# Kernel optimization log

Measured on AMD Instinct MI355X. Metric: run time of the kernel, lower is better.

## Reference

```python
import jax, jax.numpy as jnp
import numpy as np

N = 50000      # nodes
E = 800000     # edges
F = 128        # node feature dim (= output_size, residual)
H = 128        # hidden_size

def _uniform_fan_avg(key, shape):
    # VarianceScaling(scale=1.0, mode='fan_avg', distribution='uniform')
    fan_avg = (shape[0] + shape[1]) / 2.0
    limit = np.sqrt(3.0 / fan_avg)
    return jax.random.uniform(key, shape, jnp.float32, -limit, limit)

def setup_inputs() -> dict:
    key = jax.random.key(0)
    ks = jax.random.split(key, 16)
    h = jax.random.normal(ks[0], (N, F), jnp.float32)
    pos = jax.random.normal(ks[1], (N, 3), jnp.float32)
    senders = jax.random.randint(ks[2], (E,), 0, N, jnp.int32)
    receivers = jax.random.randint(ks[3], (E,), 0, N, jnp.int32)
    # edge_mlp: Linear(2F+1 -> H) silu, Linear(H -> H) silu (activate_final=True)
    eW1 = _uniform_fan_avg(ks[4], (2 * F + 1, H)); eb1 = jnp.zeros((H,), jnp.float32)
    eW2 = _uniform_fan_avg(ks[5], (H, H)); eb2 = jnp.zeros((H,), jnp.float32)
    # node_mlp: Linear(F+H -> H) silu, Linear(H -> F) (no final act)
    nW1 = _uniform_fan_avg(ks[6], (F + H, H)); nb1 = jnp.zeros((H,), jnp.float32)
    nW2 = _uniform_fan_avg(ks[7], (H, F)); nb2 = jnp.zeros((F,), jnp.float32)
    # pos_correction_mlp: Linear(H -> H) silu, Linear(H -> 1, no bias, UniformScaling(dt))
    pW1 = _uniform_fan_avg(ks[8], (H, H)); pb1 = jnp.zeros((H,), jnp.float32)
    dt = 0.001
    pW2 = jax.random.uniform(ks[9], (H, 1), jnp.float32, -dt, dt) * np.sqrt(3.0)
    return {"h": h, "pos": pos, "senders": senders, "receivers": receivers,
            "eW1": eW1, "eb1": eb1, "eW2": eW2, "eb2": eb2,
            "nW1": nW1, "nb1": nb1, "nW2": nW2, "nb2": nb2,
            "pW1": pW1, "pb1": pb1, "pW2": pW2}

def reference(h, pos, senders, receivers,
              eW1, eb1, eW2, eb2,
              nW1, nb1, nW2, nb2,
              pW1, pb1, pW2):
    n = h.shape[0]
    # _coord2radial (normalize=False)
    coord_diff = pos[senders] - pos[receivers]            # [E,3]
    radial = jnp.sum(coord_diff ** 2, axis=1, keepdims=True)  # [E,1]
    # edge update (_message): concat(h[senders], h[receivers], radial) -> edge_mlp
    msg_in = jnp.concatenate([h[senders], h[receivers], radial], axis=-1)  # [E,2F+1]
    msg = jax.nn.silu(msg_in @ eW1 + eb1)
    msg = jax.nn.silu(msg @ eW2 + eb2)                    # [E,H]
    # node update (_update): aggregate messages at receivers, node_mlp, residual
    agg = jax.ops.segment_sum(msg, receivers, num_segments=n)  # [N,H]
    x = jnp.concatenate([h, agg], axis=-1)                # [N,F+H]
    x = jax.nn.silu(x @ nW1 + nb1)
    x = x @ nW2 + nb2                                     # [N,F]
    h_new = h + x                                         # residual
    # position update (_pos_update)
    pc = jax.nn.silu(msg @ pW1 + pb1) @ pW2               # [E,1]
    trans = jnp.clip(coord_diff * pc, -100, 100)          # [E,3]
    pos_new = pos + jax.ops.segment_sum(trans, senders, num_segments=n)
    return h_new, pos_new
```

## Files before the change

### kernel.cpp

```cpp
#include <hip/hip_runtime.h>
#include <hip/hip_bf16.h>

#define NNODES 50000
#define NEDGES 800000
#define EB 1024
#define SCAN_BLOCKS 196
#define TRN_BLOCKS 448

typedef short bf16x8 __attribute__((ext_vector_type(8)));
typedef float f32x4 __attribute__((ext_vector_type(4)));
typedef unsigned short u16;
typedef unsigned int u32;

__device__ __forceinline__ u16 f2bf(float f) {
    __hip_bfloat16 b = __float2bfloat16(f);
    return *reinterpret_cast<u16*>(&b);
}
__device__ __forceinline__ float bf2f(u16 v) {
    u32 u = ((u32)v) << 16;
    return __uint_as_float(u);
}
__device__ __forceinline__ u32 pack2(float a, float b) {
    __hip_bfloat162 t = __float22bfloat162_rn(float2{a, b});
    return *reinterpret_cast<u32*>(&t);
}
__device__ __forceinline__ float fast_silu(float x) {
    float e = __builtin_amdgcn_exp2f(-1.442695040888963f * x);
    return x * __builtin_amdgcn_rcpf(1.0f + e);
}
__device__ __forceinline__ bf16x8 ld8(const u16* p) {
    return *(const bf16x8*)p;
}
__device__ __forceinline__ f32x4 mfma16(bf16x8 a, bf16x8 b, f32x4 c) {
    return __builtin_amdgcn_mfma_f32_16x16x32_bf16(a, b, c, 0, 0, 0);
}

__global__ void prep_kernel(const float* __restrict__ eW1, const float* __restrict__ eW2,
                            const float* __restrict__ pW1, const float* __restrict__ nW1,
                            const float* __restrict__ nW2,
                            u16* __restrict__ eW1T, u16* __restrict__ eW2T,
                            u16* __restrict__ pW1T, u16* __restrict__ nW1T,
                            u16* __restrict__ nW2T,
                            const int* __restrict__ rcv, int* __restrict__ counts) {
    int b = blockIdx.x;
    if (b < TRN_BLOCKS) {
        int i = b * 256 + threadIdx.x;
        const float* src; u16* dst; int K;
        if (i < 32768)      { src = eW1; dst = eW1T; K = 256; }
        else if (i < 49152) { src = eW2; dst = eW2T; K = 128; i -= 32768; }
        else if (i < 65536) { src = pW1; dst = pW1T; K = 128; i -= 49152; }
        else if (i < 98304) { src = nW1; dst = nW1T; K = 256; i -= 65536; }
        else                { src = nW2; dst = nW2T; K = 128; i -= 98304; }
        int n = i / K, k = i - n * K;
        dst[i] = f2bf(src[k * 128 + n]);
    } else {
        int e = (b - TRN_BLOCKS) * 256 + threadIdx.x;
        if (e < NEDGES) atomicAdd(&counts[rcv[e]], 1);
    }
}

__global__ __launch_bounds__(256) void gemm_p(
    const float* __restrict__ h, const u16* __restrict__ eW1T,
    const u16* __restrict__ nW1T, const float* __restrict__ eb1,
    u16* __restrict__ P)
{
    const int tid  = threadIdx.x;
    const int w    = tid >> 6;
    const int lane = tid & 63;
    const int m    = lane & 15;
    const int quad = lane >> 4;
    const int ksub = quad * 8;

    bf16x8 bw[4][6];
    float bias[6];
    #pragma unroll
    for (int cc = 0; cc < 6; cc++) {
        int C = 96 * w + 16 * cc + m;
        const u16* bp;
        if (C < 128)      { bp = eW1T + C * 256;               bias[cc] = 0.5f * eb1[C]; }
        else if (C < 256) { bp = eW1T + (C - 128) * 256 + 128; bias[cc] = 0.5f * eb1[C - 128]; }
        else              { bp = nW1T + (C - 256) * 256;       bias[cc] = 0.f; }
        #pragma unroll
        for (int t = 0; t < 4; t++) bw[t][cc] = ld8(bp + t * 32 + ksub);
    }
    const int base = blockIdx.x * 64;
    #pragma unroll
    for (int mt = 0; mt < 4; mt++) {
        int nm = base + mt * 16 + m;
        if (nm >= NNODES) nm = NNODES - 1;
        bf16x8 afr[4];
        #pragma unroll
        for (int t = 0; t < 4; t++) {
            const float* ap = h + (size_t)nm * 128 + t * 32 + ksub;
            f32x4 lo = *(const f32x4*)ap;
            f32x4 hi = *(const f32x4*)(ap + 4);
            #pragma unroll
            for (int j = 0; j < 4; j++) {
                afr[t][j]     = (short)f2bf(lo[j]);
                afr[t][4 + j] = (short)f2bf(hi[j]);
            }
        }
        f32x4 acc[6];
        #pragma unroll
        for (int cc = 0; cc < 6; cc++) acc[cc] = (f32x4){0,0,0,0};
        #pragma unroll
        for (int t = 0; t < 4; t++)
            #pragma unroll
            for (int cc = 0; cc < 6; cc++)
                acc[cc] = mfma16(afr[t], bw[t][cc], acc[cc]);
        #pragma unroll
        for (int cc = 0; cc < 6; cc++) {
            int C = 96 * w + 16 * cc + m;
            #pragma unroll
            for (int r = 0; r < 4; r++) {
                int nr = base + mt * 16 + quad * 4 + r;
                if (nr < NNODES) P[(size_t)nr * 384 + C] = f2bf(acc[cc][r] + bias[cc]);
            }
        }
    }
}

__global__ void scan1(const int* __restrict__ counts, int* __restrict__ excl,
                      int* __restrict__ blkSum) {
    __shared__ int tmp[256];
    int tx = threadIdx.x;
    int i = blockIdx.x * 256 + tx;
    int v = (i < NNODES) ? counts[i] : 0;
    tmp[tx] = v;
    __syncthreads();
    for (int off = 1; off < 256; off <<= 1) {
        int t = (tx >= off) ? tmp[tx - off] : 0;
        __syncthreads();
        tmp[tx] += t;
        __syncthreads();
    }
    if (i < NNODES) excl[i] = tmp[tx] - v;
    if (tx == 255) blkSum[blockIdx.x] = tmp[255];
}
__global__ void scan2(const int* __restrict__ blkSum, int* __restrict__ blkOff) {
    __shared__ int tmp[256];
    int tx = threadIdx.x;
    int v = (tx < SCAN_BLOCKS) ? blkSum[tx] : 0;
    tmp[tx] = v;
    __syncthreads();
    for (int off = 1; off < 256; off <<= 1) {
        int t = (tx >= off) ? tmp[tx - off] : 0;
        __syncthreads();
        tmp[tx] += t;
        __syncthreads();
    }
    if (tx < SCAN_BLOCKS) blkOff[tx] = tmp[tx] - v;
}
__global__ void scan3(const int* __restrict__ excl, const int* __restrict__ blkOff,
                      int* __restrict__ cursor) {
    int i = blockIdx.x * 256 + threadIdx.x;
    if (i < NNODES) cursor[i] = excl[i] + blkOff[blockIdx.x];
}
__global__ void scatter_kernel(const int* __restrict__ rcv, int* __restrict__ cursor,
                               int* __restrict__ perm) {
    int e = blockIdx.x * 256 + threadIdx.x;
    if (e < NEDGES) {
        int p = atomicAdd(&cursor[rcv[e]], 1);
        perm[p] = e;
    }
}

struct __align__(16) EdgeLds {
    u16   m1[64 * 136];
    u16   msg[64 * 136];
    float diff[64][4];
    float pcpart[4][64];
    float wlast[128];
    float radial[64];
    int   sndloc[64];
    int   rcvloc[64];
};

__global__ __launch_bounds__(256, 4) void edge_kernel(
    const u16* __restrict__ P, const float* __restrict__ pos,
    const int* __restrict__ snd, const int* __restrict__ rcv,
    const int* __restrict__ perm,
    const float* __restrict__ eW1last,
    const u16* __restrict__ eW2T, const float* __restrict__ eb2,
    const u16* __restrict__ pW1T, const float* __restrict__ pb1,
    const float* __restrict__ pW2,
    float* __restrict__ agg, float* __restrict__ posacc)
{
    __shared__ EdgeLds S;
    const int tid  = threadIdx.x;
    const int w    = tid >> 6;
    const int lane = tid & 63;
    const int m    = lane & 15;
    const int quad = lane >> 4;
    const int ksub = quad * 8;

    bf16x8 bw2[4][2], bp1[4][2];
    float b2v[2], pb1v[2], pw2v[2];
    #pragma unroll
    for (int cc = 0; cc < 2; cc++) {
        int col = (2 * w + cc) * 16 + m;
        #pragma unroll
        for (int t = 0; t < 4; t++) {
            bw2[t][cc] = ld8(eW2T + col * 128 + t * 32 + ksub);
            bp1[t][cc] = ld8(pW1T + col * 128 + t * 32 + ksub);
        }
        b2v[cc]  = eb2[col];
        pb1v[cc] = pb1[col];
        pw2v[cc] = pW2[col];
    }
    if (tid < 128) S.wlast[tid] = eW1last[tid];

    for (int base = blockIdx.x * 64; base < NEDGES; base += gridDim.x * 64) {
        __syncthreads();
        const int e = lane;
        int eg = perm[base + e];
        int s = snd[eg], r = rcv[eg];
        if (tid < 64) {
            S.sndloc[tid] = s; S.rcvloc[tid] = r;
            float rad = 0.f;
            #pragma unroll
            for (int c = 0; c < 3; c++) {
                float d = pos[s * 3 + c] - pos[r * 3 + c];
                S.diff[tid][c] = d;
                rad += d * d;
            }
            S.radial[tid] = rad;
        }
        __syncthreads();
        {
            float rad = S.radial[e];
            const u16* pa = P + (size_t)s * 384 + w * 32;
            const u16* pb = P + (size_t)r * 384 + 128 + w * 32;
            const int sw = e >> 3;
            #pragma unroll
            for (int k = 0; k < 4; k++) {
                bf16x8 va = ld8(pa + k * 8);
                bf16x8 vb = ld8(pb + k * 8);
                u32 pk[4];
                #pragma unroll
                for (int jj = 0; jj < 4; jj++) {
                    int col = w * 32 + k * 8 + jj * 2;
                    float2 wl = *(const float2*)&S.wlast[col];
                    float v0 = bf2f((u16)va[jj * 2])     + bf2f((u16)vb[jj * 2])     + rad * wl.x;
                    float v1 = bf2f((u16)va[jj * 2 + 1]) + bf2f((u16)vb[jj * 2 + 1]) + rad * wl.y;
                    pk[jj] = pack2(fast_silu(v0), fast_silu(v1));
                }
                int chunk = (w * 4 + k) ^ sw;
                *(uint4*)&S.m1[e * 136 + chunk * 8] =
                    make_uint4(pk[0], pk[1], pk[2], pk[3]);
            }
        }
        __syncthreads();
        #pragma unroll
        for (int mt = 0; mt < 4; mt++) {
            const int rs = mt * 2 + (m >> 3);
            const int row = mt * 16 + m;
            f32x4 acc0 = (f32x4){0,0,0,0}, acc1 = (f32x4){0,0,0,0};
            #pragma unroll
            for (int t = 0; t < 4; t++) {
                bf16x8 a = *(const bf16x8*)&S.m1[row * 136 + ((t * 4 + quad) ^ rs) * 8];
                acc0 = mfma16(a, bw2[t][0], acc0);
                acc1 = mfma16(a, bw2[t][1], acc1);
            }
            #pragma unroll
            for (int cc = 0; cc < 2; cc++) {
                f32x4 acc = cc ? acc1 : acc0;
                int col = (2 * w + cc) * 16 + m;
                #pragma unroll
                for (int rr = 0; rr < 4; rr++) {
                    int orow = mt * 16 + quad * 4 + rr;
                    S.msg[orow * 136 + col] = f2bf(fast_silu(acc[rr] + b2v[cc]));
                }
            }
        }
        __syncthreads();
        #pragma unroll
        for (int mt = 0; mt < 4; mt++) {
            f32x4 acc0 = (f32x4){0,0,0,0}, acc1 = (f32x4){0,0,0,0};
            #pragma unroll
            for (int t = 0; t < 4; t++) {
                bf16x8 a = *(const bf16x8*)&S.msg[(mt * 16 + m) * 136 + t * 32 + ksub];
                acc0 = mfma16(a, bp1[t][0], acc0);
                acc1 = mfma16(a, bp1[t][1], acc1);
            }
            float p4[4];
            #pragma unroll
            for (int rr = 0; rr < 4; rr++)
                p4[rr] = fast_silu(acc0[rr] + pb1v[0]) * pw2v[0]
                       + fast_silu(acc1[rr] + pb1v[1]) * pw2v[1];
            #pragma unroll
            for (int mask = 1; mask < 16; mask <<= 1) {
                #pragma unroll
                for (int rr = 0; rr < 4; rr++) p4[rr] += __shfl_xor(p4[rr], mask);
            }
            if (m == 0) {
                #pragma unroll
                for (int rr = 0; rr < 4; rr++)
                    S.pcpart[w][mt * 16 + quad * 4 + rr] = p4[rr];
            }
        }
        {
            int half = tid >> 7, col = tid & 127;
            int r0 = half * 32;
            float a = 0.f;
            int cur = S.rcvloc[r0];
            for (int rr = r0; rr < r0 + 32; ++rr) {
                int rc = S.rcvloc[rr];
                if (rc != cur) {
                    atomicAdd(&agg[(size_t)cur * 128 + col], a);
                    a = 0.f; cur = rc;
                }
                a += bf2f(S.msg[rr * 136 + col]);
            }
            atomicAdd(&agg[(size_t)cur * 128 + col], a);
        }
        __syncthreads();
        if (tid < 192) {
            int ee = tid / 3, c = tid - ee * 3;
            float pc = S.pcpart[0][ee] + S.pcpart[1][ee] + S.pcpart[2][ee] + S.pcpart[3][ee];
            float tr = S.diff[ee][c] * pc;
            tr = fminf(fmaxf(tr, -100.f), 100.f);
            atomicAdd(&posacc[S.sndloc[ee] * 3 + c], tr);
        }
    }
}

__global__ __launch_bounds__(256, 4) void node_kernel(
    const u16* __restrict__ P, const float* __restrict__ h,
    const float* __restrict__ agg,
    const u16* __restrict__ nW1T, const float* __restrict__ nb1,
    const u16* __restrict__ nW2T, const float* __restrict__ nb2,
    const float* __restrict__ pos, const float* __restrict__ posacc,
    float* __restrict__ out)
{
    __shared__ alignas(16) u16 m1[64 * 136];
    const int tid  = threadIdx.x;
    const int w    = tid >> 6;
    const int lane = tid & 63;
    const int m    = lane & 15;
    const int quad = lane >> 4;
    const int ksub = quad * 8;

    bf16x8 bw1[4][2], bw2[4][2];
    float b1v[2], b2v[2];
    #pragma unroll
    for (int cc = 0; cc < 2; cc++) {
        int col = (2 * w + cc) * 16 + m;
        #pragma unroll
        for (int t = 0; t < 4; t++) {
            bw1[t][cc] = ld8(nW1T + col * 256 + 128 + t * 32 + ksub);
            bw2[t][cc] = ld8(nW2T + col * 128 + t * 32 + ksub);
        }
        b1v[cc] = nb1[col];
        b2v[cc] = nb2[col];
    }
    const int base = blockIdx.x * 64;
    #pragma unroll
    for (int mt = 0; mt < 4; mt++) {
        int nm = base + mt * 16 + m;
        if (nm >= NNODES) nm = NNODES - 1;
        f32x4 acc0 = (f32x4){0,0,0,0}, acc1 = (f32x4){0,0,0,0};
        #pragma unroll
        for (int t = 0; t < 4; t++) {
            const float* ap = agg + (size_t)nm * 128 + t * 32 + ksub;
            f32x4 lo = *(const f32x4*)ap;
            f32x4 hi = *(const f32x4*)(ap + 4);
            bf16x8 a;
            #pragma unroll
            for (int j = 0; j < 4; j++) {
                a[j]     = (short)f2bf(lo[j]);
                a[4 + j] = (short)f2bf(hi[j]);
            }
            acc0 = mfma16(a, bw1[t][0], acc0);
            acc1 = mfma16(a, bw1[t][1], acc1);
        }
        #pragma unroll
        for (int cc = 0; cc < 2; cc++) {
            f32x4 acc = cc ? acc1 : acc0;
            int col = (2 * w + cc) * 16 + m;
            #pragma unroll
            for (int rr = 0; rr < 4; rr++) {
                int row = mt * 16 + quad * 4 + rr;
                int nrc = base + row; if (nrc >= NNODES) nrc = NNODES - 1;
                float v = acc[rr] + bf2f(P[(size_t)nrc * 384 + 256 + col]) + b1v[cc];
                m1[row * 136 + col] = f2bf(fast_silu(v));
            }
        }
    }
    __syncthreads();
    #pragma unroll
    for (int mt = 0; mt < 4; mt++) {
        f32x4 acc0 = (f32x4){0,0,0,0}, acc1 = (f32x4){0,0,0,0};
        #pragma unroll
        for (int t = 0; t < 4; t++) {
            bf16x8 a = *(const bf16x8*)&m1[(mt * 16 + m) * 136 + t * 32 + ksub];
            acc0 = mfma16(a, bw2[t][0], acc0);
            acc1 = mfma16(a, bw2[t][1], acc1);
        }
        #pragma unroll
        for (int cc = 0; cc < 2; cc++) {
            f32x4 acc = cc ? acc1 : acc0;
            int col = (2 * w + cc) * 16 + m;
            #pragma unroll
            for (int rr = 0; rr < 4; rr++) {
                int nr = base + mt * 16 + quad * 4 + rr;
                if (nr < NNODES)
                    out[(size_t)nr * 128 + col] = acc[rr] + b2v[cc] + h[(size_t)nr * 128 + col];
            }
        }
    }
    if (tid < 192) {
        int i = blockIdx.x * 192 + tid;
        if (i < NNODES * 3) out[NNODES * 128 + i] = pos[i] + posacc[i];
    }
}

extern "C" void kernel_launch(void* const* d_in, const int* in_sizes, int n_in,
                              void* d_out, int out_size, void* d_ws, size_t ws_size,
                              hipStream_t stream) {
    (void)in_sizes; (void)n_in; (void)out_size; (void)ws_size;
    const float* h   = (const float*)d_in[0];
    const float* pos = (const float*)d_in[1];
    const int*   snd = (const int*)d_in[2];
    const int*   rcv = (const int*)d_in[3];
    const float* eW1 = (const float*)d_in[4];
    const float* eb1 = (const float*)d_in[5];
    const float* eW2 = (const float*)d_in[6];
    const float* eb2 = (const float*)d_in[7];
    const float* nW1 = (const float*)d_in[8];
    const float* nb1 = (const float*)d_in[9];
    const float* nW2 = (const float*)d_in[10];
    const float* nb2 = (const float*)d_in[11];
    const float* pW1 = (const float*)d_in[12];
    const float* pb1 = (const float*)d_in[13];
    const float* pW2 = (const float*)d_in[14];
    float* out = (float*)d_out;

    float* agg    = (float*)d_ws;
    float* posacc = agg + (size_t)NNODES * 128;
    u16* P    = (u16*)(posacc + (size_t)NNODES * 3);
    u16* eW1T = P + (size_t)NNODES * 384;
    u16* eW2T = eW1T + 128 * 256;
    u16* pW1T = eW2T + 128 * 128;
    u16* nW1T = pW1T + 128 * 128;
    u16* nW2T = nW1T + 128 * 256;
    int* counts = (int*)(nW2T + 128 * 128);
    int* excl   = counts + 50048;
    int* blkSum = excl + 50048;
    int* blkOff = blkSum + 256;
    int* cursor = blkOff + 256;
    int* perm   = cursor + 50048;

    hipMemsetAsync(agg, 0, (size_t)NNODES * 131 * sizeof(float), stream);
    hipMemsetAsync(counts, 0, 50048 * sizeof(int), stream);

    prep_kernel<<<TRN_BLOCKS + (NEDGES + 255) / 256, 256, 0, stream>>>(
        eW1, eW2, pW1, nW1, nW2, eW1T, eW2T, pW1T, nW1T, nW2T, rcv, counts);

    gemm_p<<<(NNODES + 63) / 64, 256, 0, stream>>>(h, eW1T, nW1T, eb1, P);

    scan1<<<SCAN_BLOCKS, 256, 0, stream>>>(counts, excl, blkSum);
    scan2<<<1, 256, 0, stream>>>(blkSum, blkOff);
    scan3<<<SCAN_BLOCKS, 256, 0, stream>>>(excl, blkOff, cursor);
    scatter_kernel<<<(NEDGES + 255) / 256, 256, 0, stream>>>(rcv, cursor, perm);

    edge_kernel<<<EB, 256, 0, stream>>>(
        P, pos, snd, rcv, perm,
        eW1 + 256 * 128,
        eW2T, eb2, pW1T, pb1, pW2,
        agg, posacc);

    node_kernel<<<(NNODES + 63) / 64, 256, 0, stream>>>(
        P, h, agg, nW1T, nb1, nW2T, nb2, pos, posacc, out);
}
```

Baseline: 449.8 us.

## Merge scan kernels into chained scan, fold weight conversion into gemm, precompute segment masks

Replaces the three-kernel prefix scan with one decoupled chained scan that uses per-block flags, which removes two launches. The eW1 transpose/convert step is dropped from prep, and gemm_p instead reads the fp32 weights with strided loads and converts them per block. Workspace zeroing is merged into a single memset. In edge_kernel, segment boundaries are computed once by ballot, and messages are also stored transposed in LDS so the aggregation loop reads vectorized rows and branches on a bitmask. The chained scan spin-waits on the previous block and depends on blocks being scheduled in order, and the strided weight loads in gemm_p are less coalesced.

```diff
diff --git a/kernel.cpp b/kernel.cpp
--- a/kernel.cpp
+++ b/kernel.cpp
@@ -5,7 +5,8 @@
 #define NEDGES 800000
 #define EB 1024
 #define SCAN_BLOCKS 196
-#define TRN_BLOCKS 448
+#define TRN_BLOCKS 256
+#define GP_BLOCKS 782
 
 typedef short bf16x8 __attribute__((ext_vector_type(8)));
 typedef float f32x4 __attribute__((ext_vector_type(4)));
@@ -35,33 +36,74 @@
     return __builtin_amdgcn_mfma_f32_16x16x32_bf16(a, b, c, 0, 0, 0);
 }
 
-__global__ void prep_kernel(const float* __restrict__ eW1, const float* __restrict__ eW2,
-                            const float* __restrict__ pW1, const float* __restrict__ nW1,
-                            const float* __restrict__ nW2,
-                            u16* __restrict__ eW1T, u16* __restrict__ eW2T,
-                            u16* __restrict__ pW1T, u16* __restrict__ nW1T,
-                            u16* __restrict__ nW2T,
+__global__ void prep_kernel(const float* __restrict__ eW2, const float* __restrict__ pW1,
+                            const float* __restrict__ nW1, const float* __restrict__ nW2,
+                            u16* __restrict__ eW2T, u16* __restrict__ pW1T,
+                            u16* __restrict__ nW1bT, u16* __restrict__ nW2T,
                             const int* __restrict__ rcv, int* __restrict__ counts) {
     int b = blockIdx.x;
     if (b < TRN_BLOCKS) {
         int i = b * 256 + threadIdx.x;
-        const float* src; u16* dst; int K;
-        if (i < 32768)      { src = eW1; dst = eW1T; K = 256; }
-        else if (i < 49152) { src = eW2; dst = eW2T; K = 128; i -= 32768; }
-        else if (i < 65536) { src = pW1; dst = pW1T; K = 128; i -= 49152; }
-        else if (i < 98304) { src = nW1; dst = nW1T; K = 256; i -= 65536; }
-        else                { src = nW2; dst = nW2T; K = 128; i -= 98304; }
-        int n = i / K, k = i - n * K;
-        dst[i] = f2bf(src[k * 128 + n]);
+        int which = i >> 14, local = i & 16383;
+        int c = local >> 7, k = local & 127;
+        const float* src; u16* dst; int koff = 0;
+        if (which == 0)      { src = eW2; dst = eW2T; }
+        else if (which == 1) { src = pW1; dst = pW1T; }
+        else if (which == 2) { src = nW1; dst = nW1bT; koff = 128; }
+        else                 { src = nW2; dst = nW2T; }
+        dst[local] = f2bf(src[(koff + k) * 128 + c]);
     } else {
         int e = (b - TRN_BLOCKS) * 256 + threadIdx.x;
         if (e < NEDGES) atomicAdd(&counts[rcv[e]], 1);
     }
 }
 
+__global__ __launch_bounds__(256) void scan_chained(const int* __restrict__ counts,
+                                                    int* __restrict__ cursor,
+                                                    int* __restrict__ flags) {
+    __shared__ int stmp[256];
+    __shared__ int sprev;
+    int tx = threadIdx.x, b = blockIdx.x;
+    int i = b * 256 + tx;
+    int v = (i < NNODES) ? counts[i] : 0;
+    stmp[tx] = v;
+    __syncthreads();
+    for (int off = 1; off < 256; off <<= 1) {
+        int t = (tx >= off) ? stmp[tx - off] : 0;
+        __syncthreads();
+        stmp[tx] += t;
+        __syncthreads();
+    }
+    int incl = stmp[tx], total = stmp[255];
+    if (tx == 0) {
+        int prevsum = 0;
+        if (b > 0) {
+            int f;
+            while ((f = __hip_atomic_load(&flags[b - 1], __ATOMIC_RELAXED,
+                                          __HIP_MEMORY_SCOPE_AGENT)) == 0)
+                __builtin_amdgcn_s_sleep(2);
+            prevsum = f - 1;
+        }
+        __hip_atomic_store(&flags[b], prevsum + total + 1, __ATOMIC_RELAXED,
+                           __HIP_MEMORY_SCOPE_AGENT);
+        sprev = prevsum;
+    }
+    __syncthreads();
+    if (i < NNODES) cursor[i] = sprev + incl - v;
+}
+
+__global__ void scatter_kernel(const int* __restrict__ rcv, int* __restrict__ cursor,
+                               int* __restrict__ perm) {
+    int e = blockIdx.x * 256 + threadIdx.x;
+    if (e < NEDGES) {
+        int p = atomicAdd(&cursor[rcv[e]], 1);
+        perm[p] = e;
+    }
+}
+
 __global__ __launch_bounds__(256) void gemm_p(
-    const float* __restrict__ h, const u16* __restrict__ eW1T,
-    const u16* __restrict__ nW1T, const float* __restrict__ eb1,
+    const float* __restrict__ h, const float* __restrict__ eW1,
+    const float* __restrict__ nW1, const float* __restrict__ eb1,
     u16* __restrict__ P)
 {
     const int tid  = threadIdx.x;
@@ -76,12 +118,15 @@
     #pragma unroll
     for (int cc = 0; cc < 6; cc++) {
         int C = 96 * w + 16 * cc + m;
-        const u16* bp;
-        if (C < 128)      { bp = eW1T + C * 256;               bias[cc] = 0.5f * eb1[C]; }
-        else if (C < 256) { bp = eW1T + (C - 128) * 256 + 128; bias[cc] = 0.5f * eb1[C - 128]; }
-        else              { bp = nW1T + (C - 256) * 256;       bias[cc] = 0.f; }
-        #pragma unroll
-        for (int t = 0; t < 4; t++) bw[t][cc] = ld8(bp + t * 32 + ksub);
+        const float* src; int koff, c;
+        if (C < 128)      { src = eW1; koff = 0;   c = C;       bias[cc] = 0.5f * eb1[C]; }
+        else if (C < 256) { src = eW1; koff = 128; c = C - 128; bias[cc] = 0.5f * eb1[C - 128]; }
+        else              { src = nW1; koff = 0;   c = C - 256; bias[cc] = 0.f; }
+        #pragma unroll
+        for (int t = 0; t < 4; t++)
+            #pragma unroll
+            for (int j = 0; j < 8; j++)
+                bw[t][cc][j] = (short)f2bf(src[(koff + t * 32 + ksub + j) * 128 + c]);
     }
     const int base = blockIdx.x * 64;
     #pragma unroll
@@ -117,51 +162,6 @@
                 if (nr < NNODES) P[(size_t)nr * 384 + C] = f2bf(acc[cc][r] + bias[cc]);
             }
         }
-    }
-}
-
-__global__ void scan1(const int* __restrict__ counts, int* __restrict__ excl,
-                      int* __restrict__ blkSum) {
-    __shared__ int tmp[256];
-    int tx = threadIdx.x;
-    int i = blockIdx.x * 256 + tx;
-    int v = (i < NNODES) ? counts[i] : 0;
-    tmp[tx] = v;
-    __syncthreads();
-    for (int off = 1; off < 256; off <<= 1) {
-        int t = (tx >= off) ? tmp[tx - off] : 0;
-        __syncthreads();
-        tmp[tx] += t;
-        __syncthreads();
-    }
-    if (i < NNODES) excl[i] = tmp[tx] - v;
-    if (tx == 255) blkSum[blockIdx.x] = tmp[255];
-}
-__global__ void scan2(const int* __restrict__ blkSum, int* __restrict__ blkOff) {
-    __shared__ int tmp[256];
-    int tx = threadIdx.x;
-    int v = (tx < SCAN_BLOCKS) ? blkSum[tx] : 0;
-    tmp[tx] = v;
-    __syncthreads();
-    for (int off = 1; off < 256; off <<= 1) {
-        int t = (tx >= off) ? tmp[tx - off] : 0;
-        __syncthreads();
-        tmp[tx] += t;
-        __syncthreads();
-    }
-    if (tx < SCAN_BLOCKS) blkOff[tx] = tmp[tx] - v;
-}
-__global__ void scan3(const int* __restrict__ excl, const int* __restrict__ blkOff,
-                      int* __restrict__ cursor) {
-    int i = blockIdx.x * 256 + threadIdx.x;
-    if (i < NNODES) cursor[i] = excl[i] + blkOff[blockIdx.x];
-}
-__global__ void scatter_kernel(const int* __restrict__ rcv, int* __restrict__ cursor,
-                               int* __restrict__ perm) {
-    int e = blockIdx.x * 256 + threadIdx.x;
-    if (e < NEDGES) {
-        int p = atomicAdd(&cursor[rcv[e]], 1);
-        perm[p] = e;
     }
 }
 
@@ -174,6 +174,7 @@
     float radial[64];
     int   sndloc[64];
     int   rcvloc[64];
+    u32   segmask[2];
 };
 
 __global__ __launch_bounds__(256, 4) void edge_kernel(
@@ -212,8 +213,7 @@
 
     for (int base = blockIdx.x * 64; base < NEDGES; base += gridDim.x * 64) {
         __syncthreads();
-        const int e = lane;
-        int eg = perm[base + e];
+        int eg = perm[base + lane];
         int s = snd[eg], r = rcv[eg];
         if (tid < 64) {
             S.sndloc[tid] = s; S.rcvloc[tid] = r;
@@ -225,13 +225,16 @@
                 rad += d * d;
             }
             S.radial[tid] = rad;
+            int prevr = __shfl_up(r, 1);
+            unsigned long long bm = __ballot((lane == 0) || (r != prevr));
+            if (lane == 0) { S.segmask[0] = (u32)bm; S.segmask[1] = (u32)(bm >> 32); }
         }
         __syncthreads();
         {
-            float rad = S.radial[e];
+            float rad = S.radial[lane];
             const u16* pa = P + (size_t)s * 384 + w * 32;
             const u16* pb = P + (size_t)r * 384 + 128 + w * 32;
-            const int sw = e >> 3;
+            const int sw = lane >> 3;
             #pragma unroll
             for (int k = 0; k < 4; k++) {
                 bf16x8 va = ld8(pa + k * 8);
@@ -246,31 +249,42 @@
                     pk[jj] = pack2(fast_silu(v0), fast_silu(v1));
                 }
                 int chunk = (w * 4 + k) ^ sw;
-                *(uint4*)&S.m1[e * 136 + chunk * 8] =
+                *(uint4*)&S.m1[lane * 136 + chunk * 8] =
                     make_uint4(pk[0], pk[1], pk[2], pk[3]);
             }
         }
         __syncthreads();
+        f32x4 acc2[4][2];
         #pragma unroll
         for (int mt = 0; mt < 4; mt++) {
+            acc2[mt][0] = (f32x4){0,0,0,0};
+            acc2[mt][1] = (f32x4){0,0,0,0};
             const int rs = mt * 2 + (m >> 3);
             const int row = mt * 16 + m;
-            f32x4 acc0 = (f32x4){0,0,0,0}, acc1 = (f32x4){0,0,0,0};
             #pragma unroll
             for (int t = 0; t < 4; t++) {
                 bf16x8 a = *(const bf16x8*)&S.m1[row * 136 + ((t * 4 + quad) ^ rs) * 8];
-                acc0 = mfma16(a, bw2[t][0], acc0);
-                acc1 = mfma16(a, bw2[t][1], acc1);
-            }
+                acc2[mt][0] = mfma16(a, bw2[t][0], acc2[mt][0]);
+                acc2[mt][1] = mfma16(a, bw2[t][1], acc2[mt][1]);
+            }
+        }
+        __syncthreads();
+        #pragma unroll
+        for (int mt = 0; mt < 4; mt++) {
             #pragma unroll
             for (int cc = 0; cc < 2; cc++) {
-                f32x4 acc = cc ? acc1 : acc0;
                 int col = (2 * w + cc) * 16 + m;
-                #pragma unroll
-                for (int rr = 0; rr < 4; rr++) {
-                    int orow = mt * 16 + quad * 4 + rr;
-                    S.msg[orow * 136 + col] = f2bf(fast_silu(acc[rr] + b2v[cc]));
-                }
+                int R = mt * 16 + quad * 4;
+                float v0 = fast_silu(acc2[mt][cc][0] + b2v[cc]);
+                float v1 = fast_silu(acc2[mt][cc][1] + b2v[cc]);
+                float v2 = fast_silu(acc2[mt][cc][2] + b2v[cc]);
+                float v3 = fast_silu(acc2[mt][cc][3] + b2v[cc]);
+                S.msg[(R + 0) * 136 + col] = f2bf(v0);
+                S.msg[(R + 1) * 136 + col] = f2bf(v1);
+                S.msg[(R + 2) * 136 + col] = f2bf(v2);
+                S.msg[(R + 3) * 136 + col] = f2bf(v3);
+                uint2 pk = make_uint2(pack2(v0, v1), pack2(v2, v3));
+                *(uint2*)&S.m1[col * 68 + R] = pk;
             }
         }
         __syncthreads();
@@ -302,15 +316,21 @@
         {
             int half = tid >> 7, col = tid & 127;
             int r0 = half * 32;
+            u32 mask = S.segmask[half];
+            bf16x8 mrow[4];
+            #pragma unroll
+            for (int k = 0; k < 4; k++)
+                mrow[k] = *(const bf16x8*)&S.m1[col * 68 + r0 + k * 8];
             float a = 0.f;
             int cur = S.rcvloc[r0];
-            for (int rr = r0; rr < r0 + 32; ++rr) {
-                int rc = S.rcvloc[rr];
-                if (rc != cur) {
+            #pragma unroll
+            for (int i = 0; i < 32; i++) {
+                if (i > 0 && ((mask >> i) & 1u)) {
                     atomicAdd(&agg[(size_t)cur * 128 + col], a);
-                    a = 0.f; cur = rc;
+                    a = 0.f;
+                    cur = S.rcvloc[r0 + i];
                 }
-                a += bf2f(S.msg[rr * 136 + col]);
+                a += bf2f((u16)mrow[i >> 3][i & 7]);
             }
             atomicAdd(&agg[(size_t)cur * 128 + col], a);
         }
@@ -328,7 +348,7 @@
 __global__ __launch_bounds__(256, 4) void node_kernel(
     const u16* __restrict__ P, const float* __restrict__ h,
     const float* __restrict__ agg,
-    const u16* __restrict__ nW1T, const float* __restrict__ nb1,
+    const u16* __restrict__ nW1bT, const float* __restrict__ nb1,
     const u16* __restrict__ nW2T, const float* __restrict__ nb2,
     const float* __restrict__ pos, const float* __restrict__ posacc,
     float* __restrict__ out)
@@ -348,7 +368,7 @@
         int col = (2 * w + cc) * 16 + m;
         #pragma unroll
         for (int t = 0; t < 4; t++) {
-            bw1[t][cc] = ld8(nW1T + col * 256 + 128 + t * 32 + ksub);
+            bw1[t][cc] = ld8(nW1bT + col * 128 + t * 32 + ksub);
             bw2[t][cc] = ld8(nW2T + col * 128 + t * 32 + ksub);
         }
         b1v[cc] = nb1[col];
@@ -438,30 +458,26 @@
 
     float* agg    = (float*)d_ws;
     float* posacc = agg + (size_t)NNODES * 128;
-    u16* P    = (u16*)(posacc + (size_t)NNODES * 3);
-    u16* eW1T = P + (size_t)NNODES * 384;
-    u16* eW2T = eW1T + 128 * 256;
-    u16* pW1T = eW2T + 128 * 128;
-    u16* nW1T = pW1T + 128 * 128;
-    u16* nW2T = nW1T + 128 * 256;
-    int* counts = (int*)(nW2T + 128 * 128);
-    int* excl   = counts + 50048;
-    int* blkSum = excl + 50048;
-    int* blkOff = blkSum + 256;
-    int* cursor = blkOff + 256;
+    int* counts = (int*)(posacc + (size_t)NNODES * 3);
+    int* flags  = counts + 50048;
+    int* cursor = flags + 256;
     int* perm   = cursor + 50048;
-
-    hipMemsetAsync(agg, 0, (size_t)NNODES * 131 * sizeof(float), stream);
-    hipMemsetAsync(counts, 0, 50048 * sizeof(int), stream);
+    u16* P      = (u16*)(perm + NEDGES);
+    u16* eW2T   = P + (size_t)NNODES * 384;
+    u16* pW1T   = eW2T + 128 * 128;
+    u16* nW1bT  = pW1T + 128 * 128;
+    u16* nW2T   = nW1bT + 128 * 128;
+
+    size_t zero_bytes = ((size_t)NNODES * 131 + 50048 + 256) * sizeof(float);
+    hipMemsetAsync(agg, 0, zero_bytes, stream);
 
     prep_kernel<<<TRN_BLOCKS + (NEDGES + 255) / 256, 256, 0, stream>>>(
-        eW1, eW2, pW1, nW1, nW2, eW1T, eW2T, pW1T, nW1T, nW2T, rcv, counts);
-
-    gemm_p<<<(NNODES + 63) / 64, 256, 0, stream>>>(h, eW1T, nW1T, eb1, P);
-
-    scan1<<<SCAN_BLOCKS, 256, 0, stream>>>(counts, excl, blkSum);
-    scan2<<<1, 256, 0, stream>>>(blkSum, blkOff);
-    scan3<<<SCAN_BLOCKS, 256, 0, stream>>>(excl, blkOff, cursor);
+        eW2, pW1, nW1, nW2, eW2T, pW1T, nW1bT, nW2T, rcv, counts);
+
+    scan_chained<<<SCAN_BLOCKS, 256, 0, stream>>>(counts, cursor, flags);
+
+    gemm_p<<<GP_BLOCKS, 256, 0, stream>>>(h, eW1, nW1, eb1, P);
+
     scatter_kernel<<<(NEDGES + 255) / 256, 256, 0, stream>>>(rcv, cursor, perm);
 
     edge_kernel<<<EB, 256, 0, stream>>>(
@@ -470,6 +486,6 @@
         eW2T, eb2, pW1T, pb1, pW2,
         agg, posacc);
 
-    node_kernel<<<(NNODES + 63) / 64, 256, 0, stream>>>(
-        P, h, agg, nW1T, nb1, nW2T, nb2, pos, posacc, out);
-}
+    node_kernel<<<GP_BLOCKS, 256, 0, stream>>>(
+        P, h, agg, nW1bT, nb1, nW2T, nb2, pos, posacc, out);
+}
```

Measured after the change: 600.8 us. 33.6% more time.
